# Performance work log

Hardware: AMD Instinct MI355X
Metric: run time of the kernel (lower is better)

Reference implementation:

```python
import jax, jax.numpy as jnp
import numpy as np

NEG_SLOPE = 0.2
LN_EPS = 1e-5


def _gat_layer(x, src, dst, W, a_src, a_dst, N):
    # x: [N, Fin], W: [Fin, H*C], a_src/a_dst: [H, C]
    H, C = a_src.shape
    h = (x @ W).reshape(N, H, C)
    al_src = (h * a_src).sum(-1)  # [N, H]
    al_dst = (h * a_dst).sum(-1)  # [N, H]
    e = jax.nn.leaky_relu(al_src[src] + al_dst[dst], NEG_SLOPE)  # [E, H]
    m = jax.ops.segment_max(e, dst, num_segments=N)
    e = jnp.exp(e - m[dst])
    denom = jax.ops.segment_sum(e, dst, num_segments=N)
    alpha = e / denom[dst]  # softmax over incoming edges per dst node
    msg = h[src] * alpha[:, :, None]  # [E, H, C]
    return jax.ops.segment_sum(msg, dst, num_segments=N)  # [N, H, C]


def _layer_norm(x, g, b):
    mu = x.mean(-1, keepdims=True)
    var = ((x - mu) ** 2).mean(-1, keepdims=True)
    return (x - mu) * jax.lax.rsqrt(var + LN_EPS) * g + b


def setup_inputs() -> dict:
    key = jax.random.key(0)
    ks = jax.random.split(key, 20)
    N, E, Fin, Ch, H = 50000, 800000, 128, 64, 4
    s = lambda k, shp, sc=0.05: jax.random.normal(k, shp, dtype=jnp.float32) * sc
    return {
        "x": jax.random.normal(ks[0], (N, Fin), dtype=jnp.float32),
        "edge_index": jax.random.randint(ks[1], (2, E), 0, N, dtype=jnp.int64),
        "W1": s(ks[2], (Fin, H * Ch)),
        "att_src1": s(ks[3], (H, Ch)),
        "att_dst1": s(ks[4], (H, Ch)),
        "b1": jnp.zeros((H * Ch,), jnp.float32),
        "ln1_g": jnp.ones((H * Ch,), jnp.float32),
        "ln1_b": jnp.zeros((H * Ch,), jnp.float32),
        "W2": s(ks[5], (H * Ch, Ch)),
        "att_src2": s(ks[6], (1, Ch)),
        "att_dst2": s(ks[7], (1, Ch)),
        "b2": jnp.zeros((Ch,), jnp.float32),
        "ln2_g": jnp.ones((Ch,), jnp.float32),
        "ln2_b": jnp.zeros((Ch,), jnp.float32),
        "fc1_W": s(ks[8], (Ch, Ch // 2)),
        "fc1_b": jnp.zeros((Ch // 2,), jnp.float32),
        "fc2_W": s(ks[9], (Ch // 2, 1)),
        "fc2_b": jnp.zeros((1,), jnp.float32),
    }


def reference(x, edge_index, W1, att_src1, att_dst1, b1, ln1_g, ln1_b,
              W2, att_src2, att_dst2, b2, ln2_g, ln2_b,
              fc1_W, fc1_b, fc2_W, fc2_b):
    N = x.shape[0]
    # PyG GATConv adds self-loops by default
    loop = jnp.arange(N, dtype=edge_index.dtype)
    src = jnp.concatenate([edge_index[0], loop])
    dst = jnp.concatenate([edge_index[1], loop])

    # GAT layer 1 (heads=4, concat) + LayerNorm + ReLU (dropout is identity in eval)
    h = _gat_layer(x, src, dst, W1, att_src1, att_dst1, N).reshape(N, -1) + b1
    h = jax.nn.relu(_layer_norm(h, ln1_g, ln1_b))

    # GAT layer 2 (heads=1) + LayerNorm + ReLU
    h = _gat_layer(h, src, dst, W2, att_src2, att_dst2, N).reshape(N, -1) + b2
    h = jax.nn.relu(_layer_norm(h, ln2_g, ln2_b))

    # MLP head
    h = jax.nn.relu(h @ fc1_W + fc1_b)
    return h @ fc2_W + fc2_b  # [N, 1]
```

## Files before the change

### kernel.cpp

```cpp
#include <hip/hip_runtime.h>
#include <hip/hip_fp16.h>
#include <math.h>

#define NEG_SLOPE 0.2f
#define LN_EPS 1e-5f
#define SCCHUNK 8192
#define PADCAP 64

typedef __attribute__((ext_vector_type(8))) _Float16 half8;
typedef __attribute__((ext_vector_type(4))) _Float16 half4;
typedef __attribute__((ext_vector_type(4))) float floatx4;

static __device__ __forceinline__ float lrelu(float e) {
    return e > 0.0f ? e : NEG_SLOPE * e;
}

__global__ __launch_bounds__(256) void k_g1sc(
    const float* __restrict__ x, const float* __restrict__ W1,
    const float* __restrict__ as1, const float* __restrict__ ad1,
    _Float16* __restrict__ h1, float* __restrict__ als, float* __restrict__ ald,
    const int* __restrict__ ei, unsigned* __restrict__ cursor,
    unsigned short* __restrict__ eidx,
    int N, int E, int nsc)
{
    const int tid = threadIdx.x;

    if ((int)blockIdx.x < 8 * nsc) {
        const int g = blockIdx.x & 7;
        const int chunk = blockIdx.x >> 3;
        const unsigned basev = cursor[N];
        const int Et = E + N;
        const int i0 = chunk * SCCHUNK;
#pragma unroll 4
        for (int j = 0; j < SCCHUNK / 256; ++j) {
            int i = i0 + j * 256 + tid;
            if (i < Et) {
                int s, d;
                if (i < E) { s = ei[i]; d = ei[E + i]; } else { s = d = i - E; }
                if ((d & 7) == g) {
                    unsigned pos = atomicAdd(&cursor[d], 1u) - basev;
                    if (pos < PADCAP) eidx[(size_t)d * PADCAP + pos] = (unsigned short)s;
                }
            }
        }
        return;
    }

    const int tile = blockIdx.x - 8 * nsc;
    const int lane = tid & 63, w = tid >> 6;
    const int l15 = lane & 15, quad = lane >> 4;
    const int r_base = tile * 64;

    half8 B[4][4];
    float asv[4], adv[4];
#pragma unroll
    for (int nt = 0; nt < 4; ++nt) {
        const int n = w * 64 + nt * 16 + l15;
        asv[nt] = as1[n]; adv[nt] = ad1[n];
#pragma unroll
        for (int ks = 0; ks < 4; ++ks) {
            const int k0 = ks * 32 + quad * 8;
            half8 b;
#pragma unroll
            for (int j = 0; j < 8; ++j) b[j] = (_Float16)W1[(size_t)(k0 + j) * 256 + n];
            B[ks][nt] = b;
        }
    }

#pragma unroll
    for (int rt = 0; rt < 4; ++rt) {
        const int r0 = r_base + rt * 16;
        int m = r0 + l15; if (m >= N) m = N - 1;
        half8 A[4];
#pragma unroll
        for (int ks = 0; ks < 4; ++ks) {
            const int k0 = ks * 32 + quad * 8;
            const floatx4* xp = (const floatx4*)(x + (size_t)m * 128 + k0);
            floatx4 v0 = __builtin_nontemporal_load(xp);
            floatx4 v1 = __builtin_nontemporal_load(xp + 1);
            half8 a;
            a[0] = (_Float16)v0[0]; a[1] = (_Float16)v0[1]; a[2] = (_Float16)v0[2]; a[3] = (_Float16)v0[3];
            a[4] = (_Float16)v1[0]; a[5] = (_Float16)v1[1]; a[6] = (_Float16)v1[2]; a[7] = (_Float16)v1[3];
            A[ks] = a;
        }
        floatx4 C[4];
#pragma unroll
        for (int nt = 0; nt < 4; ++nt) C[nt] = (floatx4){0.f, 0.f, 0.f, 0.f};
#pragma unroll
        for (int ks = 0; ks < 4; ++ks)
#pragma unroll
            for (int nt = 0; nt < 4; ++nt)
                C[nt] = __builtin_amdgcn_mfma_f32_16x16x32_f16(A[ks], B[ks][nt], C[nt], 0, 0, 0);

#pragma unroll
        for (int reg = 0; reg < 4; ++reg) {
            const int row = r0 + quad * 4 + reg;
            float vs = 0.f, vd = 0.f;
#pragma unroll
            for (int nt = 0; nt < 4; ++nt) {
                float c = C[nt][reg];
                if (row < N)
                    __builtin_nontemporal_store((_Float16)c,
                        h1 + (size_t)row * 256 + w * 64 + nt * 16 + l15);
                vs += c * asv[nt]; vd += c * adv[nt];
            }
#pragma unroll
            for (int o = 1; o < 16; o <<= 1) { vs += __shfl_xor(vs, o); vd += __shfl_xor(vd, o); }
            if (l15 == 0 && row < N) { als[row * 4 + w] = vs; ald[row * 4 + w] = vd; }
        }
    }
}

__global__ __launch_bounds__(256) void k_agg1(
    const _Float16* __restrict__ h1, const float* __restrict__ als, const float* __restrict__ ald,
    const unsigned* __restrict__ cursor, const unsigned short* __restrict__ eidx,
    const float* __restrict__ b1, const float* __restrict__ g1, const float* __restrict__ be1,
    _Float16* __restrict__ hln1, int N)
{
    __shared__ float alp[4][64][4];
    const int wv = threadIdx.x >> 6, lane = threadIdx.x & 63;
    int n = blockIdx.x * 4 + wv;
    if (n >= N) n = N - 1;
    const int base = n * PADCAP;
    const unsigned basev = cursor[N];
    int deg = (int)(cursor[n] - basev); if (deg > PADCAP) deg = PADCAP;
    const float4 ad = ((const float4*)ald)[n];

    float e0 = -1e30f, e1 = -1e30f, e2 = -1e30f, e3 = -1e30f;
    if (lane < deg) {
        int src = eidx[base + lane];
        float4 a4 = ((const float4*)als)[src];
        e0 = lrelu(a4.x + ad.x);
        e1 = lrelu(a4.y + ad.y);
        e2 = lrelu(a4.z + ad.z);
        e3 = lrelu(a4.w + ad.w);
    }
    float m0 = e0, m1 = e1, m2 = e2, m3 = e3;
#pragma unroll
    for (int o = 32; o; o >>= 1) {
        m0 = fmaxf(m0, __shfl_xor(m0, o));
        m1 = fmaxf(m1, __shfl_xor(m1, o));
        m2 = fmaxf(m2, __shfl_xor(m2, o));
        m3 = fmaxf(m3, __shfl_xor(m3, o));
    }
    float p0 = __expf(e0 - m0), p1 = __expf(e1 - m1);
    float p2 = __expf(e2 - m2), p3 = __expf(e3 - m3);
    float s0 = p0, s1 = p1, s2 = p2, s3 = p3;
#pragma unroll
    for (int o = 32; o; o >>= 1) {
        s0 += __shfl_xor(s0, o);
        s1 += __shfl_xor(s1, o);
        s2 += __shfl_xor(s2, o);
        s3 += __shfl_xor(s3, o);
    }
    float4 av;
    av.x = p0 / s0; av.y = p1 / s1; av.z = p2 / s2; av.w = p3 / s3;
    *(float4*)(&alp[wv][lane][0]) = av;

    float4 acc = make_float4(0.f, 0.f, 0.f, 0.f);
    const int hd = lane >> 4, l15 = lane & 15;
    const float* alpr = &alp[wv][0][hd];
    for (int c0 = 0; c0 < deg; c0 += 16) {
        int nc = deg - c0; if (nc > 16) nc = 16;
        int j = c0 + l15; if (j >= deg) j = deg - 1;
        int srcv = eidx[base + j];
        for (int e0 = 0; e0 < nc; e0 += 4) {
#pragma unroll
            for (int u = 0; u < 4; ++u) {
                const int e = e0 + u;
                int s = __builtin_amdgcn_readlane(srcv, e);
                float a_e = alpr[(c0 + e) * 4];
                half4 v = *(const half4*)(h1 + (size_t)s * 256 + 4 * lane);
                acc.x = fmaf((float)v.x, a_e, acc.x);
                acc.y = fmaf((float)v.y, a_e, acc.y);
                acc.z = fmaf((float)v.z, a_e, acc.z);
                acc.w = fmaf((float)v.w, a_e, acc.w);
            }
        }
    }

    float4 bb = ((const float4*)b1)[lane];
    float y0 = acc.x + bb.x, y1 = acc.y + bb.y, y2 = acc.z + bb.z, y3 = acc.w + bb.w;
    float ps = y0 + y1 + y2 + y3;
    float pss = y0 * y0 + y1 * y1 + y2 * y2 + y3 * y3;
#pragma unroll
    for (int o = 32; o; o >>= 1) { ps += __shfl_xor(ps, o); pss += __shfl_xor(pss, o); }
    float mu = ps * (1.f / 256.f);
    float var = pss * (1.f / 256.f) - mu * mu;
    float rstd = rsqrtf(var + LN_EPS);
    float4 gg = ((const float4*)g1)[lane];
    float4 b2v = ((const float4*)be1)[lane];
    half4 outv;
    outv.x = (_Float16)fmaxf((y0 - mu) * rstd * gg.x + b2v.x, 0.f);
    outv.y = (_Float16)fmaxf((y1 - mu) * rstd * gg.y + b2v.y, 0.f);
    outv.z = (_Float16)fmaxf((y2 - mu) * rstd * gg.z + b2v.z, 0.f);
    outv.w = (_Float16)fmaxf((y3 - mu) * rstd * gg.w + b2v.w, 0.f);
    ((half4*)(hln1 + (size_t)n * 256))[lane] = outv;
}

__global__ __launch_bounds__(256) void k_gemm2(
    const _Float16* __restrict__ hln1, const float* __restrict__ W2,
    const float* __restrict__ as2, const float* __restrict__ ad2,
    _Float16* __restrict__ h2, float* __restrict__ als2, float* __restrict__ ald2, int N)
{
    __shared__ float ps_s[4][64], ps_d[4][64];
    const int lane = threadIdx.x & 63, w = threadIdx.x >> 6;
    const int l15 = lane & 15, quad = lane >> 4;
    const int r_base = blockIdx.x * 64;

    const int n = w * 16 + l15;
    const float asv = as2[n], adv = ad2[n];
    half8 B[8];
#pragma unroll
    for (int ks = 0; ks < 8; ++ks) {
        const int k0 = ks * 32 + quad * 8;
        half8 b;
#pragma unroll
        for (int j = 0; j < 8; ++j) b[j] = (_Float16)W2[(size_t)(k0 + j) * 64 + n];
        B[ks] = b;
    }

#pragma unroll
    for (int rt = 0; rt < 4; ++rt) {
        const int r0 = r_base + rt * 16;
        int m = r0 + l15; if (m >= N) m = N - 1;
        floatx4 C = (floatx4){0.f, 0.f, 0.f, 0.f};
#pragma unroll
        for (int ks = 0; ks < 8; ++ks) {
            half8 a = *(const half8*)(hln1 + (size_t)m * 256 + ks * 32 + quad * 8);
            C = __builtin_amdgcn_mfma_f32_16x16x32_f16(a, B[ks], C, 0, 0, 0);
        }
#pragma unroll
        for (int reg = 0; reg < 4; ++reg) {
            const int row = r0 + quad * 4 + reg;
            float c = C[reg];
            if (row < N) h2[(size_t)row * 64 + n] = (_Float16)c;
            float vs = c * asv, vd = c * adv;
#pragma unroll
            for (int o = 1; o < 16; o <<= 1) { vs += __shfl_xor(vs, o); vd += __shfl_xor(vd, o); }
            if (l15 == 0) {
                ps_s[w][rt * 16 + quad * 4 + reg] = vs;
                ps_d[w][rt * 16 + quad * 4 + reg] = vd;
            }
        }
    }
    __syncthreads();
    const int t = threadIdx.x;
    if (t < 64) {
        const int row = r_base + t;
        if (row < N) {
            als2[row] = ps_s[0][t] + ps_s[1][t] + ps_s[2][t] + ps_s[3][t];
            ald2[row] = ps_d[0][t] + ps_d[1][t] + ps_d[2][t] + ps_d[3][t];
        }
    }
}

__global__ __launch_bounds__(256) void k_agg2(
    const _Float16* __restrict__ h2, const float* __restrict__ als, const float* __restrict__ ald,
    const unsigned* __restrict__ cursor, const unsigned short* __restrict__ eidx,
    const float* __restrict__ b2, const float* __restrict__ g2, const float* __restrict__ be2,
    const float* __restrict__ fc1W, const float* __restrict__ fc1b,
    const float* __restrict__ fc2W, const float* __restrict__ fc2b,
    float* __restrict__ out, int N)
{
    __shared__ float sh[4][64];
    const int wv = threadIdx.x >> 6, lane = threadIdx.x & 63;
    int n = blockIdx.x * 4 + wv;
    if (n >= N) n = N - 1;
    const int base = n * PADCAP;
    const unsigned basev = cursor[N];
    int deg = (int)(cursor[n] - basev); if (deg > PADCAP) deg = PADCAP;
    const float adn = ald[n];

    int jj = lane < deg ? lane : deg - 1;
    int srcv = eidx[base + jj];
    float e = -1e30f;
    if (lane < deg) e = lrelu(als[srcv] + adn);
    float m = e;
#pragma unroll
    for (int o = 32; o; o >>= 1) m = fmaxf(m, __shfl_xor(m, o));
    float p = __expf(e - m);
    float s = p;
#pragma unroll
    for (int o = 32; o; o >>= 1) s += __shfl_xor(s, o);
    const float alpha = p / s;

    float acc = 0.f;
    for (int e0 = 0; e0 < deg; e0 += 4) {
#pragma unroll
        for (int u = 0; u < 4; ++u) {
            const int e2 = e0 + u;
            int sidx = __builtin_amdgcn_readlane(srcv, e2);
            float a_e = __int_as_float(
                __builtin_amdgcn_readlane(__float_as_int(alpha), e2));
            acc = fmaf((float)h2[(size_t)sidx * 64 + lane], a_e, acc);
        }
    }

    float y = acc + b2[lane];
    float ps = y, pss = y * y;
#pragma unroll
    for (int o = 32; o; o >>= 1) { ps += __shfl_xor(ps, o); pss += __shfl_xor(pss, o); }
    float mu = ps * (1.f / 64.f);
    float var = pss * (1.f / 64.f) - mu * mu;
    float r = fmaxf((y - mu) * rsqrtf(var + LN_EPS) * g2[lane] + be2[lane], 0.f);

    sh[wv][lane] = r;

    if (lane < 32) {
        float a1 = fc1b[lane];
#pragma unroll 8
        for (int k = 0; k < 64; ++k) a1 += sh[wv][k] * fc1W[k * 32 + lane];
        a1 = fmaxf(a1, 0.f);
        float t = a1 * fc2W[lane];
#pragma unroll
        for (int o = 16; o; o >>= 1) t += __shfl_xor(t, o);
        if (lane == 0) out[n] = t + fc2b[0];
    }
}

extern "C" void kernel_launch(void* const* d_in, const int* in_sizes, int n_in,
                              void* d_out, int out_size, void* d_ws, size_t ws_size,
                              hipStream_t stream)
{
    const float* x   = (const float*)d_in[0];
    const int* ei    = (const int*)d_in[1];
    const float* W1  = (const float*)d_in[2];
    const float* as1 = (const float*)d_in[3];
    const float* ad1 = (const float*)d_in[4];
    const float* b1  = (const float*)d_in[5];
    const float* g1  = (const float*)d_in[6];
    const float* be1 = (const float*)d_in[7];
    const float* W2  = (const float*)d_in[8];
    const float* as2 = (const float*)d_in[9];
    const float* ad2 = (const float*)d_in[10];
    const float* b2  = (const float*)d_in[11];
    const float* g2  = (const float*)d_in[12];
    const float* be2 = (const float*)d_in[13];
    const float* fc1W = (const float*)d_in[14];
    const float* fc1b = (const float*)d_in[15];
    const float* fc2W = (const float*)d_in[16];
    const float* fc2b = (const float*)d_in[17];
    float* out = (float*)d_out;

    const int N = in_sizes[0] / 128;
    const int E = in_sizes[1] / 2;
    const int Et = E + N;
    const int nsc = (Et + SCCHUNK - 1) / SCCHUNK;
    const int ntiles = (N + 63) / 64;

    char* p = (char*)d_ws;
    auto carve = [&](size_t bytes) {
        void* q = p;
        p += (bytes + 255) & ~(size_t)255;
        return q;
    };
    _Float16* h1    = (_Float16*)carve((size_t)N * 256 * 2);
    _Float16* hln1h = (_Float16*)carve((size_t)N * 256 * 2);
    _Float16* h2    = (_Float16*)carve((size_t)N * 64 * 2);
    float* als1 = (float*)carve((size_t)N * 4 * 4);
    float* ald1 = (float*)carve((size_t)N * 4 * 4);
    float* als2 = (float*)carve((size_t)N * 4);
    float* ald2 = (float*)carve((size_t)N * 4);
    unsigned* cursor = (unsigned*)carve((size_t)(N + 1) * 4);
    unsigned short* eidx = (unsigned short*)carve((size_t)N * PADCAP * 2);

    k_g1sc<<<8 * nsc + ntiles, 256, 0, stream>>>(x, W1, as1, ad1, h1, als1, ald1,
                                                 ei, cursor, eidx, N, E, nsc);
    k_agg1<<<(N + 3) / 4, 256, 0, stream>>>(h1, als1, ald1, cursor, eidx, b1, g1, be1, hln1h, N);
    k_gemm2<<<(N + 63) / 64, 256, 0, stream>>>(hln1h, W2, as2, ad2, h2, als2, ald2, N);
    k_agg2<<<(N + 3) / 4, 256, 0, stream>>>(h2, als2, ald2, cursor, eidx,
                                            b2, g2, be2, fc1W, fc1b, fc2W, fc2b, out, N);
}
```

Measured before the change: 321.3 us.

## Single-pass edge scatter, plain loads, and padded 8-way unrolled aggregation loops

The edge-bucketing phase now scans each chunk of edges once with a single block. Before, eight blocks each scanned the same chunk and kept only destinations matching their residue mod 8. The fp32 x loads and fp16 h1 stores in the layer-1 GEMM switch from nontemporal to ordinary accesses. In both aggregation kernels each lane loads its source index once up front, and the edge loop is padded to a multiple of 8 and fully unrolled by 8. Padded edges carry zero attention weight and a valid duplicated index. This cuts redundant edge-index reads and loop overhead, at the cost of more cross-XCD atomic contention on the cursor counters and some wasted gathers on padded edges.

```diff
diff --git a/kernel.cpp b/kernel.cpp
--- a/kernel.cpp
+++ b/kernel.cpp
@@ -25,28 +25,24 @@
 {
     const int tid = threadIdx.x;
 
-    if ((int)blockIdx.x < 8 * nsc) {
-        const int g = blockIdx.x & 7;
-        const int chunk = blockIdx.x >> 3;
+    if ((int)blockIdx.x < nsc) {
         const unsigned basev = cursor[N];
         const int Et = E + N;
-        const int i0 = chunk * SCCHUNK;
+        const int i0 = blockIdx.x * SCCHUNK;
 #pragma unroll 4
         for (int j = 0; j < SCCHUNK / 256; ++j) {
             int i = i0 + j * 256 + tid;
             if (i < Et) {
                 int s, d;
                 if (i < E) { s = ei[i]; d = ei[E + i]; } else { s = d = i - E; }
-                if ((d & 7) == g) {
-                    unsigned pos = atomicAdd(&cursor[d], 1u) - basev;
-                    if (pos < PADCAP) eidx[(size_t)d * PADCAP + pos] = (unsigned short)s;
-                }
+                unsigned pos = atomicAdd(&cursor[d], 1u) - basev;
+                if (pos < PADCAP) eidx[(size_t)d * PADCAP + pos] = (unsigned short)s;
             }
         }
         return;
     }
 
-    const int tile = blockIdx.x - 8 * nsc;
+    const int tile = blockIdx.x - nsc;
     const int lane = tid & 63, w = tid >> 6;
     const int l15 = lane & 15, quad = lane >> 4;
     const int r_base = tile * 64;
@@ -75,12 +71,11 @@
 #pragma unroll
         for (int ks = 0; ks < 4; ++ks) {
             const int k0 = ks * 32 + quad * 8;
-            const floatx4* xp = (const floatx4*)(x + (size_t)m * 128 + k0);
-            floatx4 v0 = __builtin_nontemporal_load(xp);
-            floatx4 v1 = __builtin_nontemporal_load(xp + 1);
+            const float4* xp = (const float4*)(x + (size_t)m * 128 + k0);
+            float4 v0 = xp[0], v1 = xp[1];
             half8 a;
-            a[0] = (_Float16)v0[0]; a[1] = (_Float16)v0[1]; a[2] = (_Float16)v0[2]; a[3] = (_Float16)v0[3];
-            a[4] = (_Float16)v1[0]; a[5] = (_Float16)v1[1]; a[6] = (_Float16)v1[2]; a[7] = (_Float16)v1[3];
+            a[0] = (_Float16)v0.x; a[1] = (_Float16)v0.y; a[2] = (_Float16)v0.z; a[3] = (_Float16)v0.w;
+            a[4] = (_Float16)v1.x; a[5] = (_Float16)v1.y; a[6] = (_Float16)v1.z; a[7] = (_Float16)v1.w;
             A[ks] = a;
         }
         floatx4 C[4];
@@ -99,9 +94,7 @@
 #pragma unroll
             for (int nt = 0; nt < 4; ++nt) {
                 float c = C[nt][reg];
-                if (row < N)
-                    __builtin_nontemporal_store((_Float16)c,
-                        h1 + (size_t)row * 256 + w * 64 + nt * 16 + l15);
+                if (row < N) h1[(size_t)row * 256 + w * 64 + nt * 16 + l15] = (_Float16)c;
                 vs += c * asv[nt]; vd += c * adv[nt];
             }
 #pragma unroll
@@ -126,10 +119,10 @@
     int deg = (int)(cursor[n] - basev); if (deg > PADCAP) deg = PADCAP;
     const float4 ad = ((const float4*)ald)[n];
 
+    const int srcv = eidx[base + (lane < deg ? lane : deg - 1)];
     float e0 = -1e30f, e1 = -1e30f, e2 = -1e30f, e3 = -1e30f;
     if (lane < deg) {
-        int src = eidx[base + lane];
-        float4 a4 = ((const float4*)als)[src];
+        float4 a4 = ((const float4*)als)[srcv];
         e0 = lrelu(a4.x + ad.x);
         e1 = lrelu(a4.y + ad.y);
         e2 = lrelu(a4.z + ad.z);
@@ -158,24 +151,20 @@
     *(float4*)(&alp[wv][lane][0]) = av;
 
     float4 acc = make_float4(0.f, 0.f, 0.f, 0.f);
-    const int hd = lane >> 4, l15 = lane & 15;
+    const int hd = lane >> 4;
     const float* alpr = &alp[wv][0][hd];
-    for (int c0 = 0; c0 < deg; c0 += 16) {
-        int nc = deg - c0; if (nc > 16) nc = 16;
-        int j = c0 + l15; if (j >= deg) j = deg - 1;
-        int srcv = eidx[base + j];
-        for (int e0 = 0; e0 < nc; e0 += 4) {
-#pragma unroll
-            for (int u = 0; u < 4; ++u) {
-                const int e = e0 + u;
-                int s = __builtin_amdgcn_readlane(srcv, e);
-                float a_e = alpr[(c0 + e) * 4];
-                half4 v = *(const half4*)(h1 + (size_t)s * 256 + 4 * lane);
-                acc.x = fmaf((float)v.x, a_e, acc.x);
-                acc.y = fmaf((float)v.y, a_e, acc.y);
-                acc.z = fmaf((float)v.z, a_e, acc.z);
-                acc.w = fmaf((float)v.w, a_e, acc.w);
-            }
+    const int degr = (deg + 7) & ~7;
+    for (int eb = 0; eb < degr; eb += 8) {
+#pragma unroll
+        for (int u = 0; u < 8; ++u) {
+            const int e = eb + u;
+            int s = __builtin_amdgcn_readlane(srcv, e);
+            float a_e = alpr[e * 4];
+            half4 v = *(const half4*)(h1 + (size_t)s * 256 + 4 * lane);
+            acc.x = fmaf((float)v.x, a_e, acc.x);
+            acc.y = fmaf((float)v.y, a_e, acc.y);
+            acc.z = fmaf((float)v.z, a_e, acc.z);
+            acc.w = fmaf((float)v.w, a_e, acc.w);
         }
     }
 
@@ -272,8 +261,7 @@
     int deg = (int)(cursor[n] - basev); if (deg > PADCAP) deg = PADCAP;
     const float adn = ald[n];
 
-    int jj = lane < deg ? lane : deg - 1;
-    int srcv = eidx[base + jj];
+    const int srcv = eidx[base + (lane < deg ? lane : deg - 1)];
     float e = -1e30f;
     if (lane < deg) e = lrelu(als[srcv] + adn);
     float m = e;
@@ -286,10 +274,11 @@
     const float alpha = p / s;
 
     float acc = 0.f;
-    for (int e0 = 0; e0 < deg; e0 += 4) {
-#pragma unroll
-        for (int u = 0; u < 4; ++u) {
-            const int e2 = e0 + u;
+    const int degr = (deg + 7) & ~7;
+    for (int eb = 0; eb < degr; eb += 8) {
+#pragma unroll
+        for (int u = 0; u < 8; ++u) {
+            const int e2 = eb + u;
             int sidx = __builtin_amdgcn_readlane(srcv, e2);
             float a_e = __int_as_float(
                 __builtin_amdgcn_readlane(__float_as_int(alpha), e2));
@@ -365,8 +354,8 @@
     unsigned* cursor = (unsigned*)carve((size_t)(N + 1) * 4);
     unsigned short* eidx = (unsigned short*)carve((size_t)N * PADCAP * 2);
 
-    k_g1sc<<<8 * nsc + ntiles, 256, 0, stream>>>(x, W1, as1, ad1, h1, als1, ald1,
-                                                 ei, cursor, eidx, N, E, nsc);
+    k_g1sc<<<nsc + ntiles, 256, 0, stream>>>(x, W1, as1, ad1, h1, als1, ald1,
+                                             ei, cursor, eidx, N, E, nsc);
     k_agg1<<<(N + 3) / 4, 256, 0, stream>>>(h1, als1, ald1, cursor, eidx, b1, g1, be1, hln1h, N);
     k_gemm2<<<(N + 63) / 64, 256, 0, stream>>>(hln1h, W2, as2, ad2, h2, als2, ald2, N);
     k_agg2<<<(N + 3) / 4, 256, 0, stream>>>(h2, als2, ald2, cursor, eidx,
```

Measured after the change: 277.0 us. 1.16x faster.
